# Optimization experiments

Measured on AMD Instinct MI355X. Metric: run time of the kernel, lower is better.

Reference implementation:

```python
import jax, jax.numpy as jnp
import numpy as np

N = 8192
IN_CH = 256
OUT_CH = 64
LEAKY_ALPHA = 0.5
NEG_INF = -9e15  # -9000000000000000.0 from the source


def setup_inputs() -> dict:
    key = jax.random.key(0)
    k1, k2, k3, k4 = jax.random.split(key, 4)
    h = jax.random.normal(k1, (N, IN_CH), dtype=jnp.float32)
    adj = jax.random.randint(k2, (N, N), 0, 2, dtype=jnp.int32)
    # Xavier-uniform-style init for parameters
    limW = float(np.sqrt(6.0 / (IN_CH + OUT_CH)))
    W = jax.random.uniform(k3, (IN_CH, OUT_CH), dtype=jnp.float32, minval=-limW, maxval=limW)
    lima = float(np.sqrt(6.0 / (2 * OUT_CH + 1)))
    a = jax.random.uniform(k4, (2 * OUT_CH, 1), dtype=jnp.float32, minval=-lima, maxval=lima)
    return {"h": h, "adj": adj, "W": W, "a": a}


def reference(h, adj, W, a):
    # Wh: [N, out]
    Wh = h @ W
    # additive attention score: e[i,j] = leakyrelu(Wh[i]@a1 + Wh[j]@a2)
    Wh1 = Wh @ a[:OUT_CH]   # [N, 1]
    Wh2 = Wh @ a[OUT_CH:]   # [N, 1]
    e = Wh1 + Wh2.T         # [N, N]
    e = jnp.where(e >= 0, e, LEAKY_ALPHA * e)  # LeakyReLU(0.5)
    # adjacency masking + row softmax
    att = jnp.where(adj > 0, e, jnp.float32(NEG_INF))
    att = jax.nn.softmax(att, axis=1)
    # dropout is identity in eval mode (training=False)
    h_prime = att @ Wh      # [N, out]
    # concat=True branch applies ReLU on the output
    return jax.nn.relu(h_prime)
```

## Files before the change

kernel.cpp:

```cpp
#include <hip/hip_runtime.h>
#include <stdint.h>

#define NN 8192
#define INC 256
#define OUTC 64
#define LOG2E 1.4426950408889634f

typedef __bf16 bf16x8 __attribute__((ext_vector_type(8)));
typedef float f32x4 __attribute__((ext_vector_type(4)));

__device__ __forceinline__ unsigned short f2bf(float x) {
    union { float f; unsigned u; } v; v.f = x;
    unsigned u = v.u;
    u += 0x7fffu + ((u >> 16) & 1u);
    return (unsigned short)(u >> 16);
}

#if __has_builtin(__builtin_amdgcn_exp2f)
#define EXP2(x) __builtin_amdgcn_exp2f(x)
#else
#define EXP2(x) exp2f(x)
#endif

__global__ void gat_k0(const float* __restrict__ W, const float* __restrict__ a,
                       float* __restrict__ Wa1, float* __restrict__ Wa2) {
    int k = threadIdx.x;
    float s1 = 0.f, s2 = 0.f;
    #pragma unroll 8
    for (int c = 0; c < OUTC; ++c) {
        float w = W[k * OUTC + c];
        s1 = fmaf(w, a[c], s1);
        s2 = fmaf(w, a[OUTC + c], s2);
    }
    Wa1[k] = s1; Wa2[k] = s2;
}

__global__ __launch_bounds__(256) void gat_k1(
        const float* __restrict__ h, const float* __restrict__ W,
        const float* __restrict__ Wa1, const float* __restrict__ Wa2,
        unsigned short* __restrict__ WhT, float* __restrict__ Wh1,
        float* __restrict__ Wh2) {
    __shared__ float hs[16 * INC];
    __shared__ unsigned short wt[OUTC][16];
    const int r0 = blockIdx.x * 16;
    const int t  = threadIdx.x;
    #pragma unroll
    for (int it = 0; it < 4; ++it) {
        int idx = it * 1024 + t * 4;
        float4 v = *reinterpret_cast<const float4*>(h + (size_t)r0 * INC + idx);
        hs[idx] = v.x; hs[idx + 1] = v.y; hs[idx + 2] = v.z; hs[idx + 3] = v.w;
    }
    __syncthreads();
    const int w = t >> 6, lane = t & 63;
    const int c = lane;
    const float* hr = &hs[w * 4 * INC];
    float acc0 = 0.f, acc1 = 0.f, acc2 = 0.f, acc3 = 0.f;
    #pragma unroll 8
    for (int k = 0; k < INC; ++k) {
        float wv = W[k * OUTC + c];
        acc0 = fmaf(hr[k],           wv, acc0);
        acc1 = fmaf(hr[INC + k],     wv, acc1);
        acc2 = fmaf(hr[2 * INC + k], wv, acc2);
        acc3 = fmaf(hr[3 * INC + k], wv, acc3);
    }
    float s1r[4] = {0.f, 0.f, 0.f, 0.f}, s2r[4] = {0.f, 0.f, 0.f, 0.f};
    #pragma unroll
    for (int kk = 0; kk < 4; ++kk) {
        int k = kk * 64 + lane;
        float wa1v = Wa1[k], wa2v = Wa2[k];
        #pragma unroll
        for (int r = 0; r < 4; ++r) {
            float hv = hr[r * INC + k];
            s1r[r] = fmaf(hv, wa1v, s1r[r]);
            s2r[r] = fmaf(hv, wa2v, s2r[r]);
        }
    }
    #pragma unroll
    for (int r = 0; r < 4; ++r) {
        float s1 = s1r[r], s2 = s2r[r];
        #pragma unroll
        for (int off = 32; off; off >>= 1) {
            s1 += __shfl_xor(s1, off, 64);
            s2 += __shfl_xor(s2, off, 64);
        }
        if (lane == 0) { Wh1[r0 + w * 4 + r] = s1; Wh2[r0 + w * 4 + r] = s2; }
    }
    wt[c][w * 4 + 0] = f2bf(acc0);
    wt[c][w * 4 + 1] = f2bf(acc1);
    wt[c][w * 4 + 2] = f2bf(acc2);
    wt[c][w * 4 + 3] = f2bf(acc3);
    __syncthreads();
    int cc = t >> 2, seg = t & 3;
    ushort4 v;
    v.x = wt[cc][seg * 4 + 0]; v.y = wt[cc][seg * 4 + 1];
    v.z = wt[cc][seg * 4 + 2]; v.w = wt[cc][seg * 4 + 3];
    *reinterpret_cast<ushort4*>(WhT + (size_t)cc * NN + r0 + seg * 4) = v;
}

__global__ void gat_k2(const float* __restrict__ Wh2, float* __restrict__ M) {
    __shared__ float red[4];
    int t = threadIdx.x;
    float m = -1e30f;
    for (int i = t; i < NN; i += 256) m = fmaxf(m, Wh2[i]);
    #pragma unroll
    for (int off = 32; off; off >>= 1) m = fmaxf(m, __shfl_xor(m, off, 64));
    if ((t & 63) == 0) red[t >> 6] = m;
    __syncthreads();
    if (t == 0) *M = fmaxf(fmaxf(red[0], red[1]), fmaxf(red[2], red[3]));
}

__global__ __launch_bounds__(512) void gat_k3(
        const int* __restrict__ adj, const unsigned short* __restrict__ WhT,
        const float* __restrict__ Wh1, const float* __restrict__ Wh2,
        const float* __restrict__ Mp, float* __restrict__ out) {
    __shared__ float accs[8][16 * OUTC];
    __shared__ float ls[8][16];
    const int r0 = blockIdx.x * 16;
    const int t = threadIdx.x;
    const int w = t >> 6, lane = t & 63;
    const int m = lane & 15, q = lane >> 4;
    const int row = r0 + m;
    const float wh1 = Wh1[row];
    const float Mv = *Mp;
    const float sM = wh1 + Mv;
    const float mhat = fmaxf(sM, 0.5f * sM);
    const float mh2 = mhat * LOG2E;
    const int* __restrict__ arow = adj + (size_t)row * NN;
    f32x4 acc[4] = {{0,0,0,0},{0,0,0,0},{0,0,0,0},{0,0,0,0}};
    float lpart = 0.f;

    for (int jt = w; jt < NN / 32; jt += 8) {
        const int j0 = jt * 32 + q * 8;
        int4 ai0 = *reinterpret_cast<const int4*>(arow + j0);
        int4 ai1 = *reinterpret_cast<const int4*>(arow + j0 + 4);
        float4 w20 = *reinterpret_cast<const float4*>(Wh2 + j0);
        float4 w21 = *reinterpret_cast<const float4*>(Wh2 + j0 + 4);
        float p[8];
        {
            float sv[8] = {w20.x, w20.y, w20.z, w20.w, w21.x, w21.y, w21.z, w21.w};
            int   av[8] = {ai0.x, ai0.y, ai0.z, ai0.w, ai1.x, ai1.y, ai1.z, ai1.w};
            #pragma unroll
            for (int e = 0; e < 8; ++e) {
                float s  = wh1 + sv[e];
                float lk = fmaxf(s, 0.5f * s);
                float ar = fmaf(lk, LOG2E, -mh2);
                float pe = EXP2(ar);
                p[e] = (av[e] > 0) ? pe : 0.f;
            }
        }
        lpart += ((p[0] + p[1]) + (p[2] + p[3])) + ((p[4] + p[5]) + (p[6] + p[7]));
        bf16x8 af;
        #pragma unroll
        for (int e = 0; e < 8; ++e) af[e] = (__bf16)p[e];
        #pragma unroll
        for (int ct = 0; ct < 4; ++ct) {
            const int cidx = ct * 16 + m;
            bf16x8 bfv = *reinterpret_cast<const bf16x8*>(WhT + (size_t)cidx * NN + j0);
            acc[ct] = __builtin_amdgcn_mfma_f32_16x16x32_bf16(af, bfv, acc[ct], 0, 0, 0);
        }
    }
    #pragma unroll
    for (int ct = 0; ct < 4; ++ct)
        #pragma unroll
        for (int r = 0; r < 4; ++r)
            accs[w][(q * 4 + r) * OUTC + ct * 16 + m] = acc[ct][r];
    float l = lpart;
    l += __shfl_xor(l, 16, 64);
    l += __shfl_xor(l, 32, 64);
    if (lane < 16) ls[w][lane] = l;
    __syncthreads();
    for (int e = t; e < 16 * OUTC; e += 512) {
        int rr = e >> 6, cc = e & 63;
        float s = 0.f;
        #pragma unroll
        for (int ww = 0; ww < 8; ++ww) s += accs[ww][e];
        float lsum = 0.f;
        #pragma unroll
        for (int ww = 0; ww < 8; ++ww) lsum += ls[ww][rr];
        float o = s / lsum;
        out[(size_t)(r0 + rr) * OUTC + cc] = o > 0.f ? o : 0.f;
    }
}

extern "C" void kernel_launch(void* const* d_in, const int* in_sizes, int n_in,
                              void* d_out, int out_size, void* d_ws, size_t ws_size,
                              hipStream_t stream) {
    const float* h   = (const float*)d_in[0];
    const int*   adj = (const int*)d_in[1];
    const float* W   = (const float*)d_in[2];
    const float* a   = (const float*)d_in[3];
    float* out = (float*)d_out;

    char* base = (char*)d_ws;
    float* Wa1 = (float*)(base);
    float* Wa2 = (float*)(base + 1024);
    float* Wh1 = (float*)(base + 2048);
    float* Wh2 = (float*)(base + 34816);
    float* Mp  = (float*)(base + 67584);
    unsigned short* WhT = (unsigned short*)(base + 67600);

    gat_k0<<<1, 256, 0, stream>>>(W, a, Wa1, Wa2);
    gat_k1<<<NN / 16, 256, 0, stream>>>(h, W, Wa1, Wa2, WhT, Wh1, Wh2);
    gat_k2<<<1, 256, 0, stream>>>(Wh2, Mp);
    gat_k3<<<NN / 16, 512, 0, stream>>>(adj, WhT, Wh1, Wh2, Mp, out);
}
```

Measured before the change: 456.3 us.

## Pre-swizzle Wh into MFMA fragment layout, stage Wh2 in LDS, prefetch adjacency

The projection kernel now writes Wh in a fragment-ordered layout, so each lane of the attention kernel loads its MFMA B operand contiguously instead of with a column stride of NN. The attention kernel copies Wh2 into shared memory, handles 64 columns per iteration with eight MFMAs, and prefetches the next adjacency tile into registers. The separate W·a kernel is folded into k1, with W staged in padded LDS, and the max-reduction kernel is vectorized. The cost is much more LDS per block in k1 and k3, which can lower occupancy, and W is recomputed in every k1 block.

```diff
diff --git a/kernel.cpp b/kernel.cpp
--- a/kernel.cpp
+++ b/kernel.cpp
@@ -22,33 +22,42 @@
 #define EXP2(x) exp2f(x)
 #endif
 
-__global__ void gat_k0(const float* __restrict__ W, const float* __restrict__ a,
-                       float* __restrict__ Wa1, float* __restrict__ Wa2) {
-    int k = threadIdx.x;
-    float s1 = 0.f, s2 = 0.f;
-    #pragma unroll 8
-    for (int c = 0; c < OUTC; ++c) {
-        float w = W[k * OUTC + c];
-        s1 = fmaf(w, a[c], s1);
-        s2 = fmaf(w, a[OUTC + c], s2);
-    }
-    Wa1[k] = s1; Wa2[k] = s2;
-}
-
 __global__ __launch_bounds__(256) void gat_k1(
         const float* __restrict__ h, const float* __restrict__ W,
-        const float* __restrict__ Wa1, const float* __restrict__ Wa2,
-        unsigned short* __restrict__ WhT, float* __restrict__ Wh1,
+        const float* __restrict__ a,
+        unsigned short* __restrict__ WhTf, float* __restrict__ Wh1,
         float* __restrict__ Wh2) {
+    __shared__ float Ws[256 * 65];
     __shared__ float hs[16 * INC];
+    __shared__ float Wa1s[256], Wa2s[256], as_[128];
     __shared__ unsigned short wt[OUTC][16];
     const int r0 = blockIdx.x * 16;
     const int t  = threadIdx.x;
+    if (t < 128) as_[t] = a[t];
+    #pragma unroll
+    for (int it = 0; it < 16; ++it) {
+        int idx = it * 1024 + t * 4;
+        float4 v = *reinterpret_cast<const float4*>(W + idx);
+        int k = idx >> 6, c = idx & 63;
+        float* dst = &Ws[k * 65 + c];
+        dst[0] = v.x; dst[1] = v.y; dst[2] = v.z; dst[3] = v.w;
+    }
     #pragma unroll
     for (int it = 0; it < 4; ++it) {
         int idx = it * 1024 + t * 4;
         float4 v = *reinterpret_cast<const float4*>(h + (size_t)r0 * INC + idx);
         hs[idx] = v.x; hs[idx + 1] = v.y; hs[idx + 2] = v.z; hs[idx + 3] = v.w;
+    }
+    __syncthreads();
+    {
+        float s1 = 0.f, s2 = 0.f;
+        #pragma unroll 8
+        for (int c = 0; c < OUTC; ++c) {
+            float w = Ws[t * 65 + c];
+            s1 = fmaf(w, as_[c], s1);
+            s2 = fmaf(w, as_[OUTC + c], s2);
+        }
+        Wa1s[t] = s1; Wa2s[t] = s2;
     }
     __syncthreads();
     const int w = t >> 6, lane = t & 63;
@@ -57,7 +66,7 @@
     float acc0 = 0.f, acc1 = 0.f, acc2 = 0.f, acc3 = 0.f;
     #pragma unroll 8
     for (int k = 0; k < INC; ++k) {
-        float wv = W[k * OUTC + c];
+        float wv = Ws[k * 65 + c];
         acc0 = fmaf(hr[k],           wv, acc0);
         acc1 = fmaf(hr[INC + k],     wv, acc1);
         acc2 = fmaf(hr[2 * INC + k], wv, acc2);
@@ -67,7 +76,7 @@
     #pragma unroll
     for (int kk = 0; kk < 4; ++kk) {
         int k = kk * 64 + lane;
-        float wa1v = Wa1[k], wa2v = Wa2[k];
+        float wa1v = Wa1s[k], wa2v = Wa2s[k];
         #pragma unroll
         for (int r = 0; r < 4; ++r) {
             float hv = hr[r * INC + k];
@@ -90,35 +99,59 @@
     wt[c][w * 4 + 2] = f2bf(acc2);
     wt[c][w * 4 + 3] = f2bf(acc3);
     __syncthreads();
-    int cc = t >> 2, seg = t & 3;
-    ushort4 v;
-    v.x = wt[cc][seg * 4 + 0]; v.y = wt[cc][seg * 4 + 1];
-    v.z = wt[cc][seg * 4 + 2]; v.w = wt[cc][seg * 4 + 3];
-    *reinterpret_cast<ushort4*>(WhT + (size_t)cc * NN + r0 + seg * 4) = v;
+    if (t < 128) {
+        int m = t & 15, ct = (t >> 4) & 3, oct = t >> 6;
+        int Kb = r0 >> 5;
+        int qh = (r0 >> 3) & 3;
+        int lanef = (qh + oct) * 16 + m;
+        int cidx = ct * 16 + m;
+        ushort4 v0, v1;
+        v0.x = wt[cidx][oct * 8 + 0]; v0.y = wt[cidx][oct * 8 + 1];
+        v0.z = wt[cidx][oct * 8 + 2]; v0.w = wt[cidx][oct * 8 + 3];
+        v1.x = wt[cidx][oct * 8 + 4]; v1.y = wt[cidx][oct * 8 + 5];
+        v1.z = wt[cidx][oct * 8 + 6]; v1.w = wt[cidx][oct * 8 + 7];
+        unsigned short* dst = WhTf + (((size_t)(Kb * 4 + ct)) << 9) + lanef * 8;
+        *reinterpret_cast<ushort4*>(dst)     = v0;
+        *reinterpret_cast<ushort4*>(dst + 4) = v1;
+    }
 }
 
 __global__ void gat_k2(const float* __restrict__ Wh2, float* __restrict__ M) {
-    __shared__ float red[4];
+    __shared__ float red[16];
     int t = threadIdx.x;
-    float m = -1e30f;
-    for (int i = t; i < NN; i += 256) m = fmaxf(m, Wh2[i]);
+    float4 v0 = *reinterpret_cast<const float4*>(Wh2 + t * 4);
+    float4 v1 = *reinterpret_cast<const float4*>(Wh2 + 4096 + t * 4);
+    float m = fmaxf(fmaxf(fmaxf(v0.x, v0.y), fmaxf(v0.z, v0.w)),
+                    fmaxf(fmaxf(v1.x, v1.y), fmaxf(v1.z, v1.w)));
     #pragma unroll
     for (int off = 32; off; off >>= 1) m = fmaxf(m, __shfl_xor(m, off, 64));
     if ((t & 63) == 0) red[t >> 6] = m;
     __syncthreads();
-    if (t == 0) *M = fmaxf(fmaxf(red[0], red[1]), fmaxf(red[2], red[3]));
-}
-
-__global__ __launch_bounds__(512) void gat_k3(
-        const int* __restrict__ adj, const unsigned short* __restrict__ WhT,
+    if (t == 0) {
+        float mm = red[0];
+        #pragma unroll
+        for (int i = 1; i < 16; ++i) mm = fmaxf(mm, red[i]);
+        *M = mm;
+    }
+}
+
+__global__ __launch_bounds__(512, 4) void gat_k3(
+        const int* __restrict__ adj, const unsigned short* __restrict__ WhTf,
         const float* __restrict__ Wh1, const float* __restrict__ Wh2,
         const float* __restrict__ Mp, float* __restrict__ out) {
     __shared__ float accs[8][16 * OUTC];
+    __shared__ float wh2s[NN];
     __shared__ float ls[8][16];
     const int r0 = blockIdx.x * 16;
     const int t = threadIdx.x;
     const int w = t >> 6, lane = t & 63;
     const int m = lane & 15, q = lane >> 4;
+    #pragma unroll
+    for (int it = 0; it < 4; ++it) {
+        int idx = it * 2048 + t * 4;
+        float4 v = *reinterpret_cast<const float4*>(Wh2 + idx);
+        wh2s[idx] = v.x; wh2s[idx + 1] = v.y; wh2s[idx + 2] = v.z; wh2s[idx + 3] = v.w;
+    }
     const int row = r0 + m;
     const float wh1 = Wh1[row];
     const float Mv = *Mp;
@@ -126,38 +159,68 @@
     const float mhat = fmaxf(sM, 0.5f * sM);
     const float mh2 = mhat * LOG2E;
     const int* __restrict__ arow = adj + (size_t)row * NN;
+    __syncthreads();
     f32x4 acc[4] = {{0,0,0,0},{0,0,0,0},{0,0,0,0},{0,0,0,0}};
     float lpart = 0.f;
 
-    for (int jt = w; jt < NN / 32; jt += 8) {
-        const int j0 = jt * 32 + q * 8;
-        int4 ai0 = *reinterpret_cast<const int4*>(arow + j0);
-        int4 ai1 = *reinterpret_cast<const int4*>(arow + j0 + 4);
-        float4 w20 = *reinterpret_cast<const float4*>(Wh2 + j0);
-        float4 w21 = *reinterpret_cast<const float4*>(Wh2 + j0 + 4);
-        float p[8];
-        {
-            float sv[8] = {w20.x, w20.y, w20.z, w20.w, w21.x, w21.y, w21.z, w21.w};
-            int   av[8] = {ai0.x, ai0.y, ai0.z, ai0.w, ai1.x, ai1.y, ai1.z, ai1.w};
-            #pragma unroll
-            for (int e = 0; e < 8; ++e) {
-                float s  = wh1 + sv[e];
-                float lk = fmaxf(s, 0.5f * s);
-                float ar = fmaf(lk, LOG2E, -mh2);
-                float pe = EXP2(ar);
-                p[e] = (av[e] > 0) ? pe : 0.f;
-            }
-        }
-        lpart += ((p[0] + p[1]) + (p[2] + p[3])) + ((p[4] + p[5]) + (p[6] + p[7]));
-        bf16x8 af;
-        #pragma unroll
-        for (int e = 0; e < 8; ++e) af[e] = (__bf16)p[e];
-        #pragma unroll
-        for (int ct = 0; ct < 4; ++ct) {
-            const int cidx = ct * 16 + m;
-            bf16x8 bfv = *reinterpret_cast<const bf16x8*>(WhT + (size_t)cidx * NN + j0);
-            acc[ct] = __builtin_amdgcn_mfma_f32_16x16x32_bf16(af, bfv, acc[ct], 0, 0, 0);
-        }
+    const int qo = q * 8;
+    int jt = w;
+    int4 a0 = *reinterpret_cast<const int4*>(arow + jt * 64 + qo);
+    int4 a1 = *reinterpret_cast<const int4*>(arow + jt * 64 + qo + 4);
+    int4 a2 = *reinterpret_cast<const int4*>(arow + jt * 64 + 32 + qo);
+    int4 a3 = *reinterpret_cast<const int4*>(arow + jt * 64 + 32 + qo + 4);
+
+    #pragma unroll 2
+    for (int it = 0; it < 16; ++it, jt += 8) {
+        const unsigned short* fb = WhTf + (size_t)jt * 4096 + lane * 8;
+        bf16x8 bv0 = *reinterpret_cast<const bf16x8*>(fb);
+        bf16x8 bv1 = *reinterpret_cast<const bf16x8*>(fb + 512);
+        bf16x8 bv2 = *reinterpret_cast<const bf16x8*>(fb + 1024);
+        bf16x8 bv3 = *reinterpret_cast<const bf16x8*>(fb + 1536);
+        bf16x8 bv4 = *reinterpret_cast<const bf16x8*>(fb + 2048);
+        bf16x8 bv5 = *reinterpret_cast<const bf16x8*>(fb + 2560);
+        bf16x8 bv6 = *reinterpret_cast<const bf16x8*>(fb + 3072);
+        bf16x8 bv7 = *reinterpret_cast<const bf16x8*>(fb + 3584);
+        const int jn = (it < 15) ? jt + 8 : w;
+        const int* __restrict__ anext = arow + jn * 64 + qo;
+        int4 n0 = *reinterpret_cast<const int4*>(anext);
+        int4 n1 = *reinterpret_cast<const int4*>(anext + 4);
+        int4 n2 = *reinterpret_cast<const int4*>(anext + 32);
+        int4 n3 = *reinterpret_cast<const int4*>(anext + 36);
+        const int jb = jt * 64 + qo;
+        float4 s0 = *reinterpret_cast<const float4*>(&wh2s[jb]);
+        float4 s1 = *reinterpret_cast<const float4*>(&wh2s[jb + 4]);
+        float4 s2 = *reinterpret_cast<const float4*>(&wh2s[jb + 32]);
+        float4 s3 = *reinterpret_cast<const float4*>(&wh2s[jb + 36]);
+        float sv[16] = {s0.x, s0.y, s0.z, s0.w, s1.x, s1.y, s1.z, s1.w,
+                        s2.x, s2.y, s2.z, s2.w, s3.x, s3.y, s3.z, s3.w};
+        int   av[16] = {a0.x, a0.y, a0.z, a0.w, a1.x, a1.y, a1.z, a1.w,
+                        a2.x, a2.y, a2.z, a2.w, a3.x, a3.y, a3.z, a3.w};
+        float p[16];
+        #pragma unroll
+        for (int e = 0; e < 16; ++e) {
+            float s  = wh1 + sv[e];
+            float lk = fmaxf(s, 0.5f * s);
+            float ar = fmaf(lk, LOG2E, -mh2);
+            float pe = EXP2(ar);
+            p[e] = (av[e] > 0) ? pe : 0.f;
+        }
+        float lp = 0.f;
+        #pragma unroll
+        for (int e = 0; e < 16; ++e) lp += p[e];
+        lpart += lp;
+        bf16x8 af0, af1;
+        #pragma unroll
+        for (int e = 0; e < 8; ++e) { af0[e] = (__bf16)p[e]; af1[e] = (__bf16)p[8 + e]; }
+        acc[0] = __builtin_amdgcn_mfma_f32_16x16x32_bf16(af0, bv0, acc[0], 0, 0, 0);
+        acc[1] = __builtin_amdgcn_mfma_f32_16x16x32_bf16(af0, bv1, acc[1], 0, 0, 0);
+        acc[2] = __builtin_amdgcn_mfma_f32_16x16x32_bf16(af0, bv2, acc[2], 0, 0, 0);
+        acc[3] = __builtin_amdgcn_mfma_f32_16x16x32_bf16(af0, bv3, acc[3], 0, 0, 0);
+        acc[0] = __builtin_amdgcn_mfma_f32_16x16x32_bf16(af1, bv4, acc[0], 0, 0, 0);
+        acc[1] = __builtin_amdgcn_mfma_f32_16x16x32_bf16(af1, bv5, acc[1], 0, 0, 0);
+        acc[2] = __builtin_amdgcn_mfma_f32_16x16x32_bf16(af1, bv6, acc[2], 0, 0, 0);
+        acc[3] = __builtin_amdgcn_mfma_f32_16x16x32_bf16(af1, bv7, acc[3], 0, 0, 0);
+        a0 = n0; a1 = n1; a2 = n2; a3 = n3;
     }
     #pragma unroll
     for (int ct = 0; ct < 4; ++ct)
@@ -192,15 +255,12 @@
     float* out = (float*)d_out;
 
     char* base = (char*)d_ws;
-    float* Wa1 = (float*)(base);
-    float* Wa2 = (float*)(base + 1024);
-    float* Wh1 = (float*)(base + 2048);
-    float* Wh2 = (float*)(base + 34816);
-    float* Mp  = (float*)(base + 67584);
-    unsigned short* WhT = (unsigned short*)(base + 67600);
-
-    gat_k0<<<1, 256, 0, stream>>>(W, a, Wa1, Wa2);
-    gat_k1<<<NN / 16, 256, 0, stream>>>(h, W, Wa1, Wa2, WhT, Wh1, Wh2);
-    gat_k2<<<1, 256, 0, stream>>>(Wh2, Mp);
-    gat_k3<<<NN / 16, 512, 0, stream>>>(adj, WhT, Wh1, Wh2, Mp, out);
-}
+    float* Wh1 = (float*)(base);
+    float* Wh2 = (float*)(base + 32768);
+    float* Mp  = (float*)(base + 65536);
+    unsigned short* WhTf = (unsigned short*)(base + 69632);
+
+    gat_k1<<<NN / 16, 256, 0, stream>>>(h, W, a, WhTf, Wh1, Wh2);
+    gat_k2<<<1, 1024, 0, stream>>>(Wh2, Mp);
+    gat_k3<<<NN / 16, 512, 0, stream>>>(adj, WhTf, Wh1, Wh2, Mp, out);
+}
```

Result: faster. 398.3 us (-12.7%).
